# Kernel optimization log

Hardware: AMD Instinct MI355X
Metric: run time of the kernel (lower is better)

## Reference

```python
import jax, jax.numpy as jnp
import numpy as np

VOCAB_SIZE = 1024
EMBED_DIM = 64
Z_SHAPE = (64, 32, 32, EMBED_DIM)


def setup_inputs() -> dict:
    key = jax.random.key(0)
    kz, kc = jax.random.split(key)
    z = jax.random.normal(kz, Z_SHAPE, dtype=jnp.float32)
    codebook = jax.random.uniform(kc, (VOCAB_SIZE, EMBED_DIM), dtype=jnp.float32)
    return {"z": z, "codebook": codebook}


def reference(z, codebook):
    # Flatten all leading dims: [N, D]
    z_flat = jnp.reshape(z, (-1, EMBED_DIM))
    # Squared euclidean distance via expansion: |z|^2 + |c|^2 - 2 z.c
    d1 = jnp.sum(z_flat ** 2, axis=1, keepdims=True)      # [N, 1]
    d2 = jnp.sum(codebook ** 2, axis=1)                   # [V]
    d3 = 2.0 * jnp.dot(z_flat, codebook.T)                # [N, V]
    distances = d1 + d2 - d3                              # [N, V]
    tokens = jnp.argmin(distances, axis=1)                # [N]
    tokens = jnp.reshape(tokens, z.shape[:-1])            # [B, H, W]
    z_quantized = codebook[tokens]                        # [B, H, W, D]
    return (z_quantized, tokens, codebook)
```

## Files before the change

kernel.cpp:

```cpp
#include <hip/hip_runtime.h>
#include <float.h>

constexpr int D     = 64;
constexpr int V     = 1024;
constexpr int NROWS = 65536;
constexpr float MARGIN = 0.01f;

typedef _Float16 half8 __attribute__((ext_vector_type(8)));
typedef float    f32x4 __attribute__((ext_vector_type(4)));

__global__ __launch_bounds__(256) void vq_prep(
    const float* __restrict__ cb, _Float16* __restrict__ wsH,
    _Float16* __restrict__ wsL, float* __restrict__ c2,
    float* __restrict__ cbout) {
  const int t = blockIdx.x * 256 + threadIdx.x;
#pragma unroll
  for (int i = 0; i < 16; ++i)
    ((float4*)cbout)[i * 1024 + t] = ((const float4*)cb)[i * 1024 + t];

  const int cw = t;
  const float* src = cb + (size_t)cw * D;
  float part = 0.f;
#pragma unroll
  for (int chunk = 0; chunk < 8; ++chunk) {
    float4 q0 = ((const float4*)(src + chunk * 8))[0];
    float4 q1 = ((const float4*)(src + chunk * 8))[1];
    float xs[8] = {q0.x, q0.y, q0.z, q0.w, q1.x, q1.y, q1.z, q1.w};
    half8 hh, hl;
#pragma unroll
    for (int e = 0; e < 8; ++e) {
      _Float16 hi = (_Float16)xs[e];
      hh[e] = hi;
      hl[e] = (_Float16)(xs[e] - (float)hi);
      part  = fmaf(xs[e], xs[e], part);
    }
    *(half8*)&wsH[((size_t)chunk * V + cw) * 8] = hh;
    *(half8*)&wsL[((size_t)chunk * V + cw) * 8] = hl;
  }
  c2[cw] = part;
}

__global__ __launch_bounds__(256, 6) void vq_screen(
    const float* __restrict__ z, const float* __restrict__ cb,
    const _Float16* __restrict__ wsH, const _Float16* __restrict__ wsL,
    const float* __restrict__ c2g,
    float* __restrict__ zq, float* __restrict__ tok,
    int* __restrict__ cnt, int* __restrict__ list) {
  __shared__ __align__(16) _Float16 sBh[8][64][8];
  __shared__ __align__(16) _Float16 sBl[8][64][8];
  __shared__ __align__(16) float sC2[64];
  __shared__ int   sW[4][16];
  __shared__ int   sFlagRows[64];
  __shared__ int   sFlagCnt, sFlagBase;

  const int tid  = threadIdx.x;
  const int lane = tid & 63;
  const int wv   = tid >> 6;
  const int l15  = lane & 15;
  const int quad = lane >> 4;
  const int gw   = blockIdx.x * 4 + wv;
  const int rowbase = gw * 16;

  if (tid == 0) sFlagCnt = 0;

  half8 afh[2], afl[2];
  {
    const float* zr = z + (size_t)(rowbase + l15) * D;
#pragma unroll
    for (int h = 0; h < 2; ++h) {
      const float4* p = (const float4*)(zr + h * 32 + quad * 8);
      float4 q0 = p[0], q1 = p[1];
      float xs[8] = {q0.x, q0.y, q0.z, q0.w, q1.x, q1.y, q1.z, q1.w};
      half8 ah, al;
#pragma unroll
      for (int e = 0; e < 8; ++e) {
        _Float16 hi = (_Float16)xs[e];
        ah[e] = hi;
        al[e] = (_Float16)(xs[e] - (float)hi);
      }
      afh[h] = ah; afl[h] = al;
    }
  }

  float b1[4], b2[4]; int i1[4];
#pragma unroll
  for (int r = 0; r < 4; ++r) { b1[r] = FLT_MAX; b2[r] = FLT_MAX; i1[r] = 0; }

  for (int phase = 0; phase < 16; ++phase) {
    __syncthreads();
#pragma unroll
    for (int i = 0; i < 4; ++i) {
      const int idx   = i * 256 + tid;
      const int seg   = idx >> 6;
      const int off   = idx & 63;
      const int chunk = seg & 7;
      const _Float16* srcb = (seg < 8) ? wsH : wsL;
      const half8 v = *(const half8*)&srcb[((size_t)chunk * V + phase * 64 + off) * 8];
      if (seg < 8) *(half8*)&sBh[chunk][off][0] = v;
      else         *(half8*)&sBl[chunk][off][0] = v;
    }
    if (tid < 16) {
      float4 q = ((const float4*)(c2g + phase * 64))[tid];
      *(float4*)&sC2[tid * 4] = q;
    }
    __syncthreads();
#pragma unroll 2
    for (int tl = 0; tl < 4; ++tl) {
      const int cwl  = tl * 16 + l15;
      const int vcol = phase * 64 + cwl;
      const float c2v = sC2[cwl];
      half8 bh0 = *(const half8*)&sBh[quad][cwl][0];
      half8 bh1 = *(const half8*)&sBh[4 + quad][cwl][0];
      half8 bl0 = *(const half8*)&sBl[quad][cwl][0];
      half8 bl1 = *(const half8*)&sBl[4 + quad][cwl][0];
      f32x4 acc = {0.f, 0.f, 0.f, 0.f};
      acc = __builtin_amdgcn_mfma_f32_16x16x32_f16(afh[0], bh0, acc, 0, 0, 0);
      acc = __builtin_amdgcn_mfma_f32_16x16x32_f16(afh[1], bh1, acc, 0, 0, 0);
      acc = __builtin_amdgcn_mfma_f32_16x16x32_f16(afh[0], bl0, acc, 0, 0, 0);
      acc = __builtin_amdgcn_mfma_f32_16x16x32_f16(afh[1], bl1, acc, 0, 0, 0);
      acc = __builtin_amdgcn_mfma_f32_16x16x32_f16(afl[0], bh0, acc, 0, 0, 0);
      acc = __builtin_amdgcn_mfma_f32_16x16x32_f16(afl[1], bh1, acc, 0, 0, 0);
#pragma unroll
      for (int r = 0; r < 4; ++r) {
        float m0 = fmaf(-2.f, acc[r], c2v);
        bool  c0 = m0 < b1[r];
        b2[r] = fminf(b2[r], fmaxf(m0, b1[r]));
        b1[r] = c0 ? m0 : b1[r];
        i1[r] = c0 ? vcol : i1[r];
      }
    }
  }

#pragma unroll
  for (int r = 0; r < 4; ++r) {
    float v1 = b1[r], v2 = b2[r]; int ix = i1[r];
#pragma unroll
    for (int s = 1; s < 16; s <<= 1) {
      float ov1 = __shfl_xor(v1, s);
      float ov2 = __shfl_xor(v2, s);
      int   oix = __shfl_xor(ix, s);
      bool take = (ov1 < v1) || (ov1 == v1 && oix < ix);
      float worse = take ? v1 : ov1;
      v2 = fminf(fminf(v2, ov2), worse);
      v1 = take ? ov1 : v1;
      ix = take ? oix : ix;
    }
    b1[r] = v1; b2[r] = v2; i1[r] = ix;
  }

  if (l15 == 0) {
#pragma unroll
    for (int r = 0; r < 4; ++r) {
      int rl = quad * 4 + r;
      sW[wv][rl] = i1[r];
      if (b2[r] - b1[r] < MARGIN) {
        int s = atomicAdd(&sFlagCnt, 1);
        sFlagRows[s] = rowbase + rl;
      }
    }
  }
  __syncthreads();
  if (tid == 0 && sFlagCnt > 0) sFlagBase = atomicAdd(cnt, sFlagCnt);
  __syncthreads();
  if (tid < sFlagCnt) list[sFlagBase + tid] = sFlagRows[tid];

  if (tid < 64) tok[blockIdx.x * 64 + tid] = (float)sW[tid >> 4][tid & 15];

#pragma unroll
  for (int i = 0; i < 4; ++i) {
    int cid = i * 256 + tid;
    int r = cid >> 4, seg = cid & 15;
    int widx = sW[r >> 4][r & 15];
    float4 val = *(const float4*)(cb + (size_t)widx * D + seg * 4);
    *(float4*)(zq + (size_t)(blockIdx.x * 64 + r) * D + seg * 4) = val;
  }
}

__global__ __launch_bounds__(256) void vq_fallback(
    const float* __restrict__ z, const float* __restrict__ cb,
    const int* __restrict__ cnt, const int* __restrict__ list,
    float* __restrict__ zq, float* __restrict__ tok) {
  __shared__ float sv[256];
  __shared__ int   si[256];
  const int t = threadIdx.x;
  const int n = cnt[0];
  for (int it = blockIdx.x; it < n; it += gridDim.x) {
    int row = __builtin_amdgcn_readfirstlane(list[it]);
    const float* zr = z + (size_t)row * D;
    float zreg[D];
#pragma unroll
    for (int i = 0; i < D / 4; ++i) {
      float4 q = ((const float4*)zr)[i];
      zreg[4 * i] = q.x; zreg[4 * i + 1] = q.y; zreg[4 * i + 2] = q.z; zreg[4 * i + 3] = q.w;
    }
    float d1 = 0.f;
#pragma unroll
    for (int i = 0; i < D; ++i) d1 = fmaf(zreg[i], zreg[i], d1);
    float best = FLT_MAX; int bidx = 0;
    for (int c = 0; c < 4; ++c) {
      int v = t + 256 * c;
      const float* cp = cb + (size_t)v * D;
      float acc = 0.f, cc = 0.f;
#pragma unroll
      for (int dd = 0; dd < D; ++dd) {
        acc = fmaf(zreg[dd], cp[dd], acc);
        cc  = fmaf(cp[dd], cp[dd], cc);
      }
      float dist = (d1 + cc) - 2.f * acc;
      if (dist < best) { best = dist; bidx = v; }
    }
    sv[t] = best; si[t] = bidx;
    __syncthreads();
    for (int s = 128; s > 0; s >>= 1) {
      if (t < s) {
        float v2 = sv[t + s]; int i2 = si[t + s];
        if (v2 < sv[t] || (v2 == sv[t] && i2 < si[t])) { sv[t] = v2; si[t] = i2; }
      }
      __syncthreads();
    }
    int win = si[0];
    if (t == 0) tok[row] = (float)win;
    if (t < 16) {
      float4 q = ((const float4*)(cb + (size_t)win * D))[t];
      ((float4*)(zq + (size_t)row * D))[t] = q;
    }
    __syncthreads();
  }
}

extern "C" void kernel_launch(void* const* d_in, const int* in_sizes, int n_in,
                              void* d_out, int out_size, void* d_ws, size_t ws_size,
                              hipStream_t stream) {
  const float* z  = (const float*)d_in[0];
  const float* cb = (const float*)d_in[1];

  float* out = (float*)d_out;
  float* zq  = out;
  float* tok = out + (size_t)NROWS * D;
  float* cbo = tok + NROWS;

  char* wsb = (char*)d_ws;
  _Float16* wsH  = (_Float16*)(wsb + 0);
  _Float16* wsL  = (_Float16*)(wsb + 131072);
  float*    c2   = (float*)(wsb + 262144);
  int*      cnt  = (int*)(wsb + 266240);
  int*      list = (int*)(wsb + 266496);

  hipMemsetAsync(cnt, 0, sizeof(int), stream);
  vq_prep<<<V / 256, 256, 0, stream>>>(cb, wsH, wsL, c2, cbo);
  vq_screen<<<1024, 256, 0, stream>>>(z, cb, wsH, wsL, c2, zq, tok, cnt, list);
  vq_fallback<<<1024, 256, 0, stream>>>(z, cb, cnt, list, zq, tok);
}
```

Before: 134.4 us.

## Split codebook scan across two blocks per row tile and merge in a new kernel

The screen kernel now runs twice as many blocks, each scanning half of the codebook for 64 rows, and writes per-half best, second-best and index to workspace. A new merge kernel combines the halves, writes tokens and gathered codewords, and flags near-tie rows for the fallback. The intent is more parallelism and latency hiding across the GPU. The cost is an extra launch, partial-result traffic through global memory, the z rows being loaded and converted twice, and per-row global atomics for flagged rows. The counter reset also moves from a memset into the prep kernel.

Measured after the change: 140.5 us. 1.05x slower.

```diff
diff --git a/kernel.cpp b/kernel.cpp
--- a/kernel.cpp
+++ b/kernel.cpp
@@ -12,8 +12,9 @@
 __global__ __launch_bounds__(256) void vq_prep(
     const float* __restrict__ cb, _Float16* __restrict__ wsH,
     _Float16* __restrict__ wsL, float* __restrict__ c2,
-    float* __restrict__ cbout) {
+    float* __restrict__ cbout, int* __restrict__ cnt) {
   const int t = blockIdx.x * 256 + threadIdx.x;
+  if (t == 0) cnt[0] = 0;
 #pragma unroll
   for (int i = 0; i < 16; ++i)
     ((float4*)cbout)[i * 1024 + t] = ((const float4*)cb)[i * 1024 + t];
@@ -41,27 +42,21 @@
 }
 
 __global__ __launch_bounds__(256, 6) void vq_screen(
-    const float* __restrict__ z, const float* __restrict__ cb,
+    const float* __restrict__ z,
     const _Float16* __restrict__ wsH, const _Float16* __restrict__ wsL,
     const float* __restrict__ c2g,
-    float* __restrict__ zq, float* __restrict__ tok,
-    int* __restrict__ cnt, int* __restrict__ list) {
+    float* __restrict__ pB1, float* __restrict__ pB2, int* __restrict__ pI1) {
   __shared__ __align__(16) _Float16 sBh[8][64][8];
   __shared__ __align__(16) _Float16 sBl[8][64][8];
   __shared__ __align__(16) float sC2[64];
-  __shared__ int   sW[4][16];
-  __shared__ int   sFlagRows[64];
-  __shared__ int   sFlagCnt, sFlagBase;
 
   const int tid  = threadIdx.x;
   const int lane = tid & 63;
   const int wv   = tid >> 6;
   const int l15  = lane & 15;
   const int quad = lane >> 4;
-  const int gw   = blockIdx.x * 4 + wv;
-  const int rowbase = gw * 16;
-
-  if (tid == 0) sFlagCnt = 0;
+  const int half = blockIdx.x & 1;
+  const int rowbase = (blockIdx.x >> 1) * 64 + wv * 16;
 
   half8 afh[2], afl[2];
   {
@@ -86,7 +81,8 @@
 #pragma unroll
   for (int r = 0; r < 4; ++r) { b1[r] = FLT_MAX; b2[r] = FLT_MAX; i1[r] = 0; }
 
-  for (int phase = 0; phase < 16; ++phase) {
+  for (int pp = 0; pp < 8; ++pp) {
+    const int phase = half * 8 + pp;
     __syncthreads();
 #pragma unroll
     for (int i = 0; i < 4; ++i) {
@@ -151,28 +147,46 @@
   if (l15 == 0) {
 #pragma unroll
     for (int r = 0; r < 4; ++r) {
-      int rl = quad * 4 + r;
-      sW[wv][rl] = i1[r];
-      if (b2[r] - b1[r] < MARGIN) {
-        int s = atomicAdd(&sFlagCnt, 1);
-        sFlagRows[s] = rowbase + rl;
-      }
-    }
+      const int grow = rowbase + quad * 4 + r;
+      pB1[half * NROWS + grow] = b1[r];
+      pB2[half * NROWS + grow] = b2[r];
+      pI1[half * NROWS + grow] = i1[r];
+    }
+  }
+}
+
+__global__ __launch_bounds__(256) void vq_merge(
+    const float* __restrict__ pB1, const float* __restrict__ pB2,
+    const int* __restrict__ pI1, const float* __restrict__ cb,
+    float* __restrict__ zq, float* __restrict__ tok,
+    int* __restrict__ cnt, int* __restrict__ list) {
+  __shared__ int sWin[256];
+  const int tid = threadIdx.x;
+  const int row = blockIdx.x * 256 + tid;
+
+  float v1a = pB1[row];         float v2a = pB2[row];         int ixa = pI1[row];
+  float v1b = pB1[NROWS + row]; float v2b = pB2[NROWS + row]; int ixb = pI1[NROWS + row];
+  bool take  = (v1b < v1a) || (v1b == v1a && ixb < ixa);
+  float worse = take ? v1a : v1b;
+  float v2 = fminf(fminf(v2a, v2b), worse);
+  float v1 = take ? v1b : v1a;
+  int   ix = take ? ixb : ixa;
+
+  tok[row]  = (float)ix;
+  sWin[tid] = ix;
+  if (v2 - v1 < MARGIN) {
+    int s = atomicAdd(cnt, 1);
+    list[s] = row;
   }
   __syncthreads();
-  if (tid == 0 && sFlagCnt > 0) sFlagBase = atomicAdd(cnt, sFlagCnt);
-  __syncthreads();
-  if (tid < sFlagCnt) list[sFlagBase + tid] = sFlagRows[tid];
-
-  if (tid < 64) tok[blockIdx.x * 64 + tid] = (float)sW[tid >> 4][tid & 15];
-
-#pragma unroll
-  for (int i = 0; i < 4; ++i) {
+
+  const int rb = blockIdx.x * 256;
+#pragma unroll
+  for (int i = 0; i < 16; ++i) {
     int cid = i * 256 + tid;
     int r = cid >> 4, seg = cid & 15;
-    int widx = sW[r >> 4][r & 15];
-    float4 val = *(const float4*)(cb + (size_t)widx * D + seg * 4);
-    *(float4*)(zq + (size_t)(blockIdx.x * 64 + r) * D + seg * 4) = val;
+    float4 val = *(const float4*)(cb + (size_t)sWin[r] * D + seg * 4);
+    *(float4*)(zq + (size_t)(rb + r) * D + seg * 4) = val;
   }
 }
 
@@ -245,9 +259,12 @@
   float*    c2   = (float*)(wsb + 262144);
   int*      cnt  = (int*)(wsb + 266240);
   int*      list = (int*)(wsb + 266496);
-
-  hipMemsetAsync(cnt, 0, sizeof(int), stream);
-  vq_prep<<<V / 256, 256, 0, stream>>>(cb, wsH, wsL, c2, cbo);
-  vq_screen<<<1024, 256, 0, stream>>>(z, cb, wsH, wsL, c2, zq, tok, cnt, list);
+  float*    pB1  = (float*)(wsb + 1048576);
+  float*    pB2  = (float*)(wsb + 1572864);
+  int*      pI1  = (int*)(wsb + 2097152);
+
+  vq_prep<<<V / 256, 256, 0, stream>>>(cb, wsH, wsL, c2, cbo, cnt);
+  vq_screen<<<2048, 256, 0, stream>>>(z, wsH, wsL, c2, pB1, pB2, pI1);
+  vq_merge<<<NROWS / 256, 256, 0, stream>>>(pB1, pB2, pI1, cb, zq, tok, cnt, list);
   vq_fallback<<<1024, 256, 0, stream>>>(z, cb, cnt, list, zq, tok);
 }
```
